# Performance work log

Hardware: AMD Instinct MI355X
Metric: run time of the kernel (lower is better)

Reference implementation:

```python
import jax, jax.numpy as jnp
import numpy as np

N_QUBITS = 8
N_QLAYERS = 2
D_MODEL = 8
NUM_HEADS = 2
DEPTH = D_MODEL // NUM_HEADS


def _apply_1q(state, U, wire):
    # state: (T, 2, 2, ..., 2); U: (2, 2) complex
    state = jnp.moveaxis(state, 1 + wire, -1)
    state = jnp.einsum('...b,ab->...a', state, U)
    return jnp.moveaxis(state, -1, 1 + wire)


def _apply_cnot(state, ctrl, tgt):
    s = jnp.moveaxis(state, (1 + ctrl, 1 + tgt), (-2, -1))
    s = jnp.concatenate([s[..., :1, :], s[..., 1:, ::-1]], axis=-2)
    return jnp.moveaxis(s, (-2, -1), (1 + ctrl, 1 + tgt))


def _z_signs(n):
    idx = jnp.arange(2 ** n)
    bits = (idx[:, None] >> jnp.arange(n - 1, -1, -1)[None, :]) & 1  # col i = qubit i
    return (1.0 - 2.0 * bits).astype(jnp.float32)  # (2^n, n)


def quantum_circuit(x, w):
    """AngleEmbedding(RX) + BasicEntanglerLayers(RX + CNOT ring) + PauliZ expvals.
    x: (T, n) float angles; w: (L, n) float weights -> (T, n) float expvals."""
    T, n = x.shape
    L = w.shape[0]
    # AngleEmbedding: RX(x_i)|0> = cos(x_i/2)|0> - i sin(x_i/2)|1>; product state
    h = 0.5 * x
    amps = jnp.stack([jnp.cos(h).astype(jnp.complex64),
                      (-1j) * jnp.sin(h).astype(jnp.complex64)], axis=-1)  # (T, n, 2)
    state = amps[:, 0, :]
    for i in range(1, n):
        state = (state[:, :, None] * amps[:, i, None, :]).reshape(T, -1)
    state = state.reshape((T,) + (2,) * n)
    for l in range(L):
        for i in range(n):
            th = 0.5 * w[l, i]
            cc = jnp.cos(th).astype(jnp.complex64)
            ss = (-1j) * jnp.sin(th).astype(jnp.complex64)
            U = jnp.stack([jnp.stack([cc, ss]), jnp.stack([ss, cc])])  # RX(w)
            state = _apply_1q(state, U, i)
        pairs = [(i, (i + 1) % n) for i in range(n)] if n > 2 else [(0, 1)]
        for c, t in pairs:
            state = _apply_cnot(state, c, t)
    probs = jnp.abs(state.reshape(T, -1)) ** 2  # (T, 2^n)
    return probs @ _z_signs(n)  # (T, n)


def setup_inputs() -> dict:
    key = jax.random.key(0)
    ks = jax.random.split(key, 8)
    B, S, d = 32, 1024, D_MODEL
    q = jax.random.normal(ks[0], (B, S, d), dtype=jnp.float32)
    k = jax.random.normal(ks[1], (B, S, d), dtype=jnp.float32)
    v = jax.random.normal(ks[2], (B, S, d), dtype=jnp.float32)
    mask = jnp.triu(jnp.ones((S, S), dtype=jnp.float32), k=1)[None, None]  # causal
    weights_q = jax.random.uniform(ks[3], (N_QLAYERS, N_QUBITS), dtype=jnp.float32, maxval=2 * np.pi)
    weights_k = jax.random.uniform(ks[4], (N_QLAYERS, N_QUBITS), dtype=jnp.float32, maxval=2 * np.pi)
    weights_v = jax.random.uniform(ks[5], (N_QLAYERS, N_QUBITS), dtype=jnp.float32, maxval=2 * np.pi)
    weights_dense = jax.random.uniform(ks[6], (N_QLAYERS, N_QUBITS), dtype=jnp.float32, maxval=2 * np.pi)
    return {"q": q, "k": k, "v": v, "mask": mask,
            "weights_q": weights_q, "weights_k": weights_k,
            "weights_v": weights_v, "weights_dense": weights_dense}


def reference(q, k, v, mask, weights_q, weights_k, weights_v, weights_dense):
    B, S, d = q.shape
    T = B * S
    # per-token quantum Q/K/V embeddings (batched over all B*S tokens)
    qe = quantum_circuit(q.reshape(T, d), weights_q).reshape(B, S, d)
    ke = quantum_circuit(k.reshape(T, d), weights_k).reshape(B, S, d)
    ve = quantum_circuit(v.reshape(T, d), weights_v).reshape(B, S, d)
    # split heads: (B, H, S, depth)
    def split(x):
        return x.reshape(B, S, NUM_HEADS, DEPTH).transpose(0, 2, 1, 3)
    qh, kh, vh = split(qe), split(ke), split(ve)
    scores = jnp.einsum('bhqd,bhkd->bhqk', qh, kh) / jnp.sqrt(jnp.float32(DEPTH))
    scores = scores + mask * (-1e9)
    attn = jax.nn.softmax(scores, axis=-1)
    ctx = jnp.einsum('bhqk,bhkd->bhqd', attn, vh)
    ctx = ctx.transpose(0, 2, 1, 3).reshape(B, S, d)
    out = quantum_circuit(ctx.reshape(T, d), weights_dense).reshape(B, S, d)
    return out, attn
```

## Files before the change

### kernel.cpp

```cpp
#include <hip/hip_runtime.h>

#define S_LEN 1024
#define BATCH 32
#define NHEAD 2
#define HDIM  4


#define TBL_STRIDE 256

__global__ __launch_bounds__(256)
void pauli_setup(const float* __restrict__ wq, const float* __restrict__ wk,
                 const float* __restrict__ wv, const float* __restrict__ wd,
                 float4* __restrict__ tables, int* __restrict__ counts)
{
    int blk = blockIdx.x;
    int set = blk >> 3, w = blk & 7;
    const float* wt = (set == 0) ? wq : (set == 1) ? wk : (set == 2) ? wv : wd;

    float c2[8], s2[8];
#pragma unroll
    for (int j = 0; j < 8; ++j) {
        float th = wt[8 + j];
        s2[j] = __sinf(th);
        c2[j] = __cosf(th);
    }

    unsigned X = 0u, Z = 1u << w;
    int sg0 = 0;
#pragma unroll
    for (int g = 7; g >= 0; --g) {
        int c = g, t = (g + 1) & 7;
        unsigned xc = (X >> c) & 1u, zt = (Z >> t) & 1u;
        unsigned xt = (X >> t) & 1u, zc = (Z >> c) & 1u;
        sg0 ^= (int)(xc & zt & (xt ^ zc ^ 1u));
        X ^= xc << t;
        Z ^= zt << c;
    }

    int tid = threadIdx.x;
    float coef = sg0 ? -1.0f : 1.0f;
    unsigned Xb = X;
    int k = 0;
#pragma unroll
    for (int j = 0; j < 8; ++j) {
        if ((Z >> j) & 1u) {
            int bit = (tid >> k) & 1;
            ++k;
            if (!((X >> j) & 1u)) {
                if (bit) { Xb |= 1u << j; coef *= s2[j]; }
                else     { coef *= c2[j]; }
            } else {
                if (bit) { Xb &= ~(1u << j); coef *= -s2[j]; }
                else     { coef *= c2[j]; }
            }
        }
    }
    bool valid = (tid < (1 << k));

    unsigned Xf = Xb, Zf = Z;
    int sg = 0;
#pragma unroll
    for (int g = 7; g >= 0; --g) {
        int c = g, t = (g + 1) & 7;
        unsigned xc = (Xf >> c) & 1u, zt = (Zf >> t) & 1u;
        unsigned xt = (Xf >> t) & 1u, zc = (Zf >> c) & 1u;
        sg ^= (int)(xc & zt & (xt ^ zc ^ 1u));
        Xf ^= xc << t;
        Zf ^= zt << c;
    }

    bool keep = valid && ((Xf & ~Zf) == 0u);
    if (sg ^ (__popc(Xf) & 1)) coef = -coef;
    unsigned zonly = Zf & ~Xf;
    unsigned ymask = Xf;

    __shared__ int wsum[4];
    int lane = tid & 63, wvx = tid >> 6;
    unsigned long long mb = __ballot((int)keep);
    if (lane == 0) wsum[wvx] = __popcll(mb);
    __syncthreads();
    int prefix = 0;
#pragma unroll
    for (int i = 0; i < 4; ++i)
        if (i < wvx) prefix += wsum[i];
    int pos = prefix + __popcll(mb & ((1ull << lane) - 1ull));
    if (keep) {
        float4 t4;
        t4.x = __int_as_float((int)zonly);
        t4.y = __int_as_float((int)ymask);
        t4.z = coef;
        t4.w = 0.0f;
        tables[blk * TBL_STRIDE + pos] = t4;
    }
    __syncthreads();
    if (tid == 0) counts[blk] = wsum[0] + wsum[1] + wsum[2] + wsum[3];
}

__global__ __launch_bounds__(256)
void qc_eval(const float* __restrict__ x0, const float* __restrict__ w0a,
             const float* __restrict__ x1, const float* __restrict__ w0b,
             const float* __restrict__ x2, const float* __restrict__ w0c,
             const float4* __restrict__ tables, const int* __restrict__ counts,
             float* __restrict__ o0, float* __restrict__ o1, float* __restrict__ o2,
             int rows_per_seg, int set_base)
{
    int gr = blockIdx.x * 256 + threadIdx.x;
    int seg = gr / rows_per_seg;
    int row = gr - seg * rows_per_seg;
    const float* x  = (seg == 0) ? x0 : (seg == 1) ? x1 : x2;
    const float* w0 = (seg == 0) ? w0a : (seg == 1) ? w0b : w0c;
    float*       o  = (seg == 0) ? o0 : (seg == 1) ? o1 : o2;
    int set = set_base + seg;

    const float4* xp = reinterpret_cast<const float4*>(x + (size_t)row * 8);
    float4 xa = xp[0], xb = xp[1];
    float cc[8], ss[8];
    {
        float a;
        a = xa.x + w0[0]; __sincosf(a, &ss[0], &cc[0]);
        a = xa.y + w0[1]; __sincosf(a, &ss[1], &cc[1]);
        a = xa.z + w0[2]; __sincosf(a, &ss[2], &cc[2]);
        a = xa.w + w0[3]; __sincosf(a, &ss[3], &cc[3]);
        a = xb.x + w0[4]; __sincosf(a, &ss[4], &cc[4]);
        a = xb.y + w0[5]; __sincosf(a, &ss[5], &cc[5]);
        a = xb.z + w0[6]; __sincosf(a, &ss[6], &cc[6]);
        a = xb.w + w0[7]; __sincosf(a, &ss[7], &cc[7]);
    }

    float res[8];
#pragma unroll
    for (int w = 0; w < 8; ++w) {
        int blk = set * 8 + w;
        int cnt = counts[blk];
        const float4* base = tables + blk * TBL_STRIDE;
        float acc = 0.0f;
        for (int t = 0; t < cnt; ++t) {
            float4 T = base[t];
            unsigned zm = (unsigned)__float_as_int(T.x);
            unsigned ym = (unsigned)__float_as_int(T.y);
            float v = T.z;
#pragma unroll
            for (int m = 0; m < 8; ++m) {
                float f = ((ym >> m) & 1u) ? ss[m]
                        : (((zm >> m) & 1u) ? cc[m] : 1.0f);
                v *= f;
            }
            acc += v;
        }
        res[w] = acc;
    }

    float4* op = reinterpret_cast<float4*>(o + (size_t)row * 8);
    op[0] = make_float4(res[0], res[1], res[2], res[3]);
    op[1] = make_float4(res[4], res[5], res[6], res[7]);
}

template <int CTRL>
__device__ __forceinline__ float dpp_acc(float x)
{
    int y = __builtin_amdgcn_update_dpp(0, __float_as_int(x), CTRL, 0xf, 0xf, false);
    return x + __int_as_float(y);
}

__device__ __forceinline__ float wave_reduce63(float x)
{
    x = dpp_acc<0x111>(x);
    x = dpp_acc<0x112>(x);
    x = dpp_acc<0x114>(x);
    x = dpp_acc<0x118>(x);
    x = dpp_acc<0x142>(x);
    x = dpp_acc<0x143>(x);
    return x;
}

__device__ __forceinline__ float bcast63(float x)
{
    return __int_as_float(__builtin_amdgcn_readlane(__float_as_int(x), 63));
}

__global__ __launch_bounds__(256)
void attn_kernel(const float* qe, const float* __restrict__ ke,
                 const float* __restrict__ ve, float* __restrict__ attn,
                 float* ctx)
{
    __shared__ float4 kc[4][S_LEN / 4];
    __shared__ float4 vc[4][S_LEN / 4];

    int tid = threadIdx.x;
    int bid = blockIdx.x;
    int it  = bid & 15;
    int h   = (bid >> 4) & 1;
    int b   = bid >> 5;
    int lane = tid & 63;
    int wave = tid >> 6;

    const float4* ke4 = reinterpret_cast<const float4*>(ke) + h;
    const float4* ve4 = reinterpret_cast<const float4*>(ve) + h;
    size_t rowbase = (size_t)b * S_LEN;

    for (int j = tid; j < S_LEN; j += 256) {
        kc[j & 3][j >> 2] = ke4[(rowbase + j) * 2];
        vc[j & 3][j >> 2] = ve4[(rowbase + j) * 2];
    }
    __syncthreads();

    int i0 = it * 64 + wave * 16;
    const float* qp = qe + (rowbase + i0) * 8 + h * HDIM;
    float4* attn4 = reinterpret_cast<float4*>(attn);
    size_t head4 = ((size_t)(b * NHEAD + h)) * S_LEN * (S_LEN / 4);

    for (int pr = 0; pr < 8; ++pr) {
        int i = i0 + pr * 2;

        float4 qa = *reinterpret_cast<const float4*>(qp + pr * 16);
        float4 qb = *reinterpret_cast<const float4*>(qp + pr * 16 + 8);
        qa.x *= 0.5f; qa.y *= 0.5f; qa.z *= 0.5f; qa.w *= 0.5f;
        qb.x *= 0.5f; qb.y *= 0.5f; qb.z *= 0.5f; qb.w *= 0.5f;

        float pea[16], peb[16];
        float suma = 0.0f, sumb = 0.0f;
        float4 pva = {0, 0, 0, 0}, pvb = {0, 0, 0, 0};

#pragma unroll
        for (int t = 0; t < 4; ++t) {
            int m = t * 64 + lane;
            int jb = m << 2;
#pragma unroll
            for (int c = 0; c < 4; ++c) {
                float4 kk = kc[c][m];
                float4 vv = vc[c][m];
                float sa = qa.x * kk.x + qa.y * kk.y + qa.z * kk.z + qa.w * kk.w;
                float sb = qb.x * kk.x + qb.y * kk.y + qb.z * kk.z + qb.w * kk.w;
                int j = jb + c;
                float pa = (j <= i)     ? __expf(sa) : 0.0f;
                float pb = (j <= i + 1) ? __expf(sb) : 0.0f;
                pea[t * 4 + c] = pa;
                peb[t * 4 + c] = pb;
                suma += pa; sumb += pb;
                pva.x += pa * vv.x; pva.y += pa * vv.y;
                pva.z += pa * vv.z; pva.w += pa * vv.w;
                pvb.x += pb * vv.x; pvb.y += pb * vv.y;
                pvb.z += pb * vv.z; pvb.w += pb * vv.w;
            }
        }

        float inva = 1.0f / bcast63(wave_reduce63(suma));
        float invb = 1.0f / bcast63(wave_reduce63(sumb));

        size_t base4 = head4 + (size_t)i * (S_LEN / 4) + lane;
#pragma unroll
        for (int t = 0; t < 4; ++t) {
            float4 oa, ob;
            oa.x = pea[t * 4 + 0] * inva; oa.y = pea[t * 4 + 1] * inva;
            oa.z = pea[t * 4 + 2] * inva; oa.w = pea[t * 4 + 3] * inva;
            ob.x = peb[t * 4 + 0] * invb; ob.y = peb[t * 4 + 1] * invb;
            ob.z = peb[t * 4 + 2] * invb; ob.w = peb[t * 4 + 3] * invb;
            attn4[base4 + t * 64] = oa;
            attn4[base4 + (S_LEN / 4) + t * 64] = ob;
        }

        pva.x = wave_reduce63(pva.x); pva.y = wave_reduce63(pva.y);
        pva.z = wave_reduce63(pva.z); pva.w = wave_reduce63(pva.w);
        pvb.x = wave_reduce63(pvb.x); pvb.y = wave_reduce63(pvb.y);
        pvb.z = wave_reduce63(pvb.z); pvb.w = wave_reduce63(pvb.w);

        if (lane == 63) {
            float* cp = ctx + (rowbase + i) * 8 + h * HDIM;
            cp[0]  = pva.x * inva; cp[1]  = pva.y * inva;
            cp[2]  = pva.z * inva; cp[3]  = pva.w * inva;
            cp[8]  = pvb.x * invb; cp[9]  = pvb.y * invb;
            cp[10] = pvb.z * invb; cp[11] = pvb.w * invb;
        }
    }
}

extern "C" void kernel_launch(void* const* d_in, const int* in_sizes, int n_in,
                              void* d_out, int out_size, void* d_ws, size_t ws_size,
                              hipStream_t stream)
{
    const float* q  = (const float*)d_in[0];
    const float* k  = (const float*)d_in[1];
    const float* v  = (const float*)d_in[2];
    const float* wq = (const float*)d_in[4];
    const float* wk = (const float*)d_in[5];
    const float* wv = (const float*)d_in[6];
    const float* wd = (const float*)d_in[7];

    float* out  = (float*)d_out;
    float* attn = out + (size_t)BATCH * S_LEN * 8;

    float*  ws     = (float*)d_ws;
    float*  qe     = ws;
    float*  ke     = ws + 262144;
    float*  ve     = ws + 524288;
    float4* tables = (float4*)(ws + 786432);
    int*    counts = (int*)(ws + 786432 + 32768);

    const int rows = BATCH * S_LEN;

    pauli_setup<<<dim3(32), 256, 0, stream>>>(wq, wk, wv, wd, tables, counts);

    qc_eval<<<dim3(rows * 3 / 256), 256, 0, stream>>>(
        q, wq, k, wk, v, wv, tables, counts, qe, ke, ve, rows, 0);

    attn_kernel<<<dim3(BATCH * NHEAD * 16), 256, 0, stream>>>(qe, ke, ve, attn, qe);

    qc_eval<<<dim3(rows / 256), 256, 0, stream>>>(
        qe, wd, qe, wd, qe, wd, tables, counts, out, out, out, rows, 3);
}
```

Measured before the change: 91.42 us.

## Split qc_eval outputs across four threads per row, add nontemporal attn stores

qc_eval now assigns four threads per row, each computing two of the eight Pauli expectation values. Wires are paired so that per-thread work (table term counts) is roughly balanced, which raises parallelism and shortens the per-thread serial loop. Each thread still recomputes the eight sincos values and does a scalar store. The attention kernel writes its large attn matrix with nontemporal stores to avoid cache pollution, and staggers each wave's row order so concurrent waves spread their accesses.

```diff
diff --git a/kernel.cpp b/kernel.cpp
--- a/kernel.cpp
+++ b/kernel.cpp
@@ -4,6 +4,8 @@
 #define BATCH 32
 #define NHEAD 2
 #define HDIM  4
+
+typedef float vfloat4 __attribute__((ext_vector_type(4)));
 
 
 #define TBL_STRIDE 256
@@ -104,9 +106,11 @@
              float* __restrict__ o0, float* __restrict__ o1, float* __restrict__ o2,
              int rows_per_seg, int set_base)
 {
-    int gr = blockIdx.x * 256 + threadIdx.x;
-    int seg = gr / rows_per_seg;
-    int row = gr - seg * rows_per_seg;
+    int gtid = blockIdx.x * 256 + threadIdx.x;
+    int rowg = gtid >> 2;
+    int op   = gtid & 3;
+    int seg  = rowg / rows_per_seg;
+    int row  = rowg - seg * rows_per_seg;
     const float* x  = (seg == 0) ? x0 : (seg == 1) ? x1 : x2;
     const float* w0 = (seg == 0) ? w0a : (seg == 1) ? w0b : w0c;
     float*       o  = (seg == 0) ? o0 : (seg == 1) ? o1 : o2;
@@ -127,9 +131,13 @@
         a = xb.w + w0[7]; __sincosf(a, &ss[7], &cc[7]);
     }
 
-    float res[8];
-#pragma unroll
-    for (int w = 0; w < 8; ++w) {
+    const int wA4[4] = {0, 2, 3, 4};
+    const int wB4[4] = {1, 7, 6, 5};
+    int wA = wA4[op], wB = wB4[op];
+
+#pragma unroll
+    for (int half = 0; half < 2; ++half) {
+        int w = half ? wB : wA;
         int blk = set * 8 + w;
         int cnt = counts[blk];
         const float4* base = tables + blk * TBL_STRIDE;
@@ -147,12 +155,8 @@
             }
             acc += v;
         }
-        res[w] = acc;
-    }
-
-    float4* op = reinterpret_cast<float4*>(o + (size_t)row * 8);
-    op[0] = make_float4(res[0], res[1], res[2], res[3]);
-    op[1] = make_float4(res[4], res[5], res[6], res[7]);
+        o[(size_t)row * 8 + w] = acc;
+    }
 }
 
 template <int CTRL>
@@ -178,6 +182,12 @@
     return __int_as_float(__builtin_amdgcn_readlane(__float_as_int(x), 63));
 }
 
+__device__ __forceinline__ void nt_store4(float4 v, float4* p)
+{
+    vfloat4 nv = { v.x, v.y, v.z, v.w };
+    __builtin_nontemporal_store(nv, reinterpret_cast<vfloat4*>(p));
+}
+
 __global__ __launch_bounds__(256)
 void attn_kernel(const float* qe, const float* __restrict__ ke,
                  const float* __restrict__ ve, float* __restrict__ attn,
@@ -209,7 +219,8 @@
     float4* attn4 = reinterpret_cast<float4*>(attn);
     size_t head4 = ((size_t)(b * NHEAD + h)) * S_LEN * (S_LEN / 4);
 
-    for (int pr = 0; pr < 8; ++pr) {
+    for (int prr = 0; prr < 8; ++prr) {
+        int pr = (prr + wave * 2) & 7;
         int i = i0 + pr * 2;
 
         float4 qa = *reinterpret_cast<const float4*>(qp + pr * 16);
@@ -255,8 +266,8 @@
             oa.z = pea[t * 4 + 2] * inva; oa.w = pea[t * 4 + 3] * inva;
             ob.x = peb[t * 4 + 0] * invb; ob.y = peb[t * 4 + 1] * invb;
             ob.z = peb[t * 4 + 2] * invb; ob.w = peb[t * 4 + 3] * invb;
-            attn4[base4 + t * 64] = oa;
-            attn4[base4 + (S_LEN / 4) + t * 64] = ob;
+            nt_store4(oa, &attn4[base4 + t * 64]);
+            nt_store4(ob, &attn4[base4 + (S_LEN / 4) + t * 64]);
         }
 
         pva.x = wave_reduce63(pva.x); pva.y = wave_reduce63(pva.y);
@@ -300,11 +311,11 @@
 
     pauli_setup<<<dim3(32), 256, 0, stream>>>(wq, wk, wv, wd, tables, counts);
 
-    qc_eval<<<dim3(rows * 3 / 256), 256, 0, stream>>>(
+    qc_eval<<<dim3(rows * 3 * 4 / 256), 256, 0, stream>>>(
         q, wq, k, wk, v, wv, tables, counts, qe, ke, ve, rows, 0);
 
     attn_kernel<<<dim3(BATCH * NHEAD * 16), 256, 0, stream>>>(qe, ke, ve, attn, qe);
 
-    qc_eval<<<dim3(rows / 256), 256, 0, stream>>>(
+    qc_eval<<<dim3(rows * 4 / 256), 256, 0, stream>>>(
         qe, wd, qe, wd, qe, wd, tables, counts, out, out, out, rows, 3);
 }
```

Measured after the change: 96.24 us. +5.3%, slower.
